# Kernel optimization log

Hardware: AMD Instinct MI355X
Metric: run time of the kernel (lower is better)

The kernel has to match this reference:

```python
import jax, jax.numpy as jnp
import numpy as np
import math

M = 512          # num_bin_x
NB = 512         # num_bin_y
NUM_NODES = 2_000_000
K = 4            # max bins a node can overlap per dim (size <= 2.5 bins)
SQRT2 = math.sqrt(2.0)


def setup_inputs() -> dict:
    key = jax.random.key(0)
    k1, k2 = jax.random.split(key)
    node_pos = jax.random.uniform(k1, (NUM_NODES, 2), jnp.float32, 0.05, 0.95)
    # node sizes between 0.5 and 2.5 bins (normalized layout units)
    node_size = jax.random.uniform(k2, (NUM_NODES, 2), jnp.float32) * (2.0 / M) + (0.5 / M)
    return {
        "node_pos": node_pos,
        "node_size": node_size,
        "node_weight": jnp.ones((NUM_NODES,), jnp.float32),
        "expand_ratio": jnp.ones((NUM_NODES,), jnp.float32),
        "unit_len": jnp.array([1.0 / M, 1.0 / NB], jnp.float32),
        "init_density_map": jnp.zeros((M, NB), jnp.float32),
        "num_bin_x": M,
        "num_bin_y": NB,
    }


def pre_normalize(node_pos, node_size, node_weight, expand_ratio, unit_len, mx, ny):
    # density_map_cuda.pre_normalize: expand tiny nodes to sqrt(2)*unit_len,
    # rescale weight to preserve area, convert rects to bin coordinates.
    ux, uy = unit_len[0], unit_len[1]
    w, h = node_size[:, 0], node_size[:, 1]
    new_w = jnp.maximum(w, SQRT2 * ux)
    new_h = jnp.maximum(h, SQRT2 * uy)
    weight = node_weight * expand_ratio * (w * h) / (new_w * new_h)
    xl = jnp.clip((node_pos[:, 0] - 0.5 * new_w) / ux, 0.0, mx)
    xh = jnp.clip((node_pos[:, 0] + 0.5 * new_w) / ux, 0.0, mx)
    yl = jnp.clip((node_pos[:, 1] - 0.5 * new_h) / uy, 0.0, ny)
    yh = jnp.clip((node_pos[:, 1] + 0.5 * new_h) / uy, 0.0, ny)
    return jnp.stack([xl, xh, yl, yh, weight], axis=1)  # [N, 5]


def scatter_density(info, mx, ny):
    # density_map_cuda.forward: overlap-area scatter-add of node rects into bins.
    xl, xh, yl, yh, w = info[:, 0], info[:, 1], info[:, 2], info[:, 3], info[:, 4]
    bx0 = jnp.floor(xl).astype(jnp.int32)
    by0 = jnp.floor(yl).astype(jnp.int32)
    dm = jnp.zeros((mx, ny), jnp.float32)
    for dx in range(K):
        ix = bx0 + dx
        fx = ix.astype(jnp.float32)
        ox = jnp.clip(jnp.minimum(xh, fx + 1.0) - jnp.maximum(xl, fx), 0.0)
        ixc = jnp.clip(ix, 0, mx - 1)
        for dy in range(K):
            iy = by0 + dy
            fy = iy.astype(jnp.float32)
            oy = jnp.clip(jnp.minimum(yh, fy + 1.0) - jnp.maximum(yl, fy), 0.0)
            iyc = jnp.clip(iy, 0, ny - 1)
            dm = dm.at[ixc, iyc].add(w * ox * oy)
    return dm


def make_transforms(n):
    k = jnp.arange(n, dtype=jnp.float32)[:, None]
    m = jnp.arange(n, dtype=jnp.float32)[None, :]
    ang = jnp.pi * k * (2.0 * m + 1.0) / (2.0 * n)
    C = jnp.cos(ang)  # [freq, space]
    S = jnp.sin(ang)
    w = jnp.where(jnp.arange(n) == 0, 1.0, 2.0).astype(jnp.float32)
    return C, S, w


def spectral_solve(dm, unit_len, mx, ny):
    # fft_scale construction from __init__
    wj = (jnp.arange(mx, dtype=jnp.float32) * (2.0 * jnp.pi / mx))[:, None]
    wk = (jnp.arange(ny, dtype=jnp.float32) * (2.0 * jnp.pi / ny))[None, :]
    wk = wk * (unit_len[0] / unit_len[1])  # scale_w_k=True
    wsq = wj ** 2 + wk ** 2
    wsq = wsq.at[0, 0].set(1.0)
    pscale = (1.0 / wsq).at[0, 0].set(0.0)
    fx_scale = wj * pscale * 0.5
    fy_scale = wk * pscale * 0.5

    Cx, Sx, wx = make_transforms(mx)
    Cy, Sy, wy = make_transforms(ny)
    # dct2: coeff[u,v] = (1/(M*N)) * sum_{m,n} dm[m,n] cos(pi u(2m+1)/2M) cos(pi v(2n+1)/2N)
    coeff = (Cx @ dm @ Cy.T) / (mx * ny)
    ICx = (wx[:, None] * Cx)  # weighted inverse cosine basis [freq, space]
    ICy = (wy[:, None] * Cy)
    ISx = (wx[:, None] * Sx)
    ISy = (wy[:, None] * Sy)
    potential = ICx.T @ (coeff * pscale) @ ICy          # idct2
    force_x = ISx.T @ (coeff * fx_scale) @ ICy          # idxst_idct
    force_y = ICx.T @ (coeff * fy_scale) @ ISy          # idct_idxst
    return potential, force_x, force_y


def reference(node_pos, node_size, node_weight, expand_ratio, unit_len,
              init_density_map, num_bin_x, num_bin_y):
    info = pre_normalize(node_pos, node_size, node_weight, expand_ratio,
                         unit_len, num_bin_x, num_bin_y)
    density_map = init_density_map + scatter_density(info, num_bin_x, num_bin_y)
    potential, _, _ = spectral_solve(density_map, unit_len, num_bin_x, num_bin_y)
    energy = jnp.sum(potential * density_map)
    return energy
```

## Files before the change

### kernel.cpp

```cpp
#include <hip/hip_runtime.h>
#include <math.h>

#define MX 512
#define NY 512
#define TWO_PI 6.283185307179586f

#define TSHIFT 6
#define NT 64
#define LDIM 68
#define SLAB (LDIM * LDIM)
#define SLAB4 (SLAB / 4)
#define NPB 2048
#define KPT 8
#define CAP 40960
#define TTARGET 1216
#define RPARTS 19
#define QSCALE 26214.0f
#define QINV (1.0f / 26214.0f)

typedef __attribute__((ext_vector_type(8))) short short8;
typedef __attribute__((ext_vector_type(4))) float float4_t;
typedef __attribute__((ext_vector_type(4))) unsigned short ushort4_t;

__device__ __forceinline__ unsigned short f2bf(float x) {
    union { float f; unsigned u; } v; v.f = x;
    unsigned r = v.u + 0x7fffu + ((v.u >> 16) & 1u);
    return (unsigned short)(r >> 16);
}
__device__ __forceinline__ float bf2f(unsigned short h) {
    union { float f; unsigned u; } v; v.u = ((unsigned)h) << 16;
    return v.f;
}

__device__ __forceinline__ void node_bounds(float2 p, float2 s, float ux, float uy,
                                            float& xl, float& xh, float& yl, float& yh,
                                            float& nw, float& nh) {
    const float SQ2 = 1.41421356237309515f;
    nw = fmaxf(s.x, SQ2 * ux);
    nh = fmaxf(s.y, SQ2 * uy);
    xl = fminf(fmaxf((p.x - 0.5f * nw) / ux, 0.0f), (float)MX);
    xh = fminf(fmaxf((p.x + 0.5f * nw) / ux, 0.0f), (float)MX);
    yl = fminf(fmaxf((p.y - 0.5f * nh) / uy, 0.0f), (float)NY);
    yh = fminf(fmaxf((p.y + 0.5f * nh) / uy, 0.0f), (float)NY);
}

__global__ void gen_cos_kernel(unsigned short* __restrict__ Ch,
                               unsigned short* __restrict__ Cl,
                               unsigned int* __restrict__ base,
                               unsigned int* __restrict__ cursor,
                               float* __restrict__ out, int cap_mode) {
    int idx = blockIdx.x * blockDim.x + threadIdx.x;
    if (idx == 0) *out = 0.0f;
    if (cap_mode && idx <= NT) {
        base[idx] = (unsigned int)idx * CAP;
        if (idx < NT) cursor[idx] = (unsigned int)idx * CAP;
    }
    int a = idx >> 9;
    int j = idx & 511;
    float x = cospif((float)(a * (2 * j + 1)) * (1.0f / 1024.0f));
    unsigned short hi = f2bf(x);
    Ch[idx] = hi;
    Cl[idx] = f2bf(x - bf2f(hi));
}

__global__ __launch_bounds__(256)
void count_kernel(const float2* __restrict__ pos, const float2* __restrict__ size,
                  const float* __restrict__ unit_len,
                  unsigned int* __restrict__ cnt, int n) {
    __shared__ unsigned int h[NT];
    if (threadIdx.x < NT) h[threadIdx.x] = 0;
    __syncthreads();
    float ux = unit_len[0], uy = unit_len[1];
    int start = blockIdx.x * NPB;
    int end = min(start + NPB, n);
#pragma unroll
    for (int k = 0; k < KPT; k++) {
        int i = start + k * 256 + (int)threadIdx.x;
        if (i < end) {
            float xl, xh, yl, yh, nw, nh;
            node_bounds(pos[i], size[i], ux, uy, xl, xh, yl, yh, nw, nh);
            int bx0 = min((int)floorf(xl), MX - 1);
            int by0 = min((int)floorf(yl), NY - 1);
            atomicAdd(&h[((bx0 >> TSHIFT) << 3) | (by0 >> TSHIFT)], 1u);
        }
    }
    __syncthreads();
    if (threadIdx.x < NT) {
        unsigned int c = h[threadIdx.x];
        if (c) atomicAdd(&cnt[threadIdx.x], c);
    }
}

__global__ void scan_kernel(const unsigned int* __restrict__ cnt,
                            unsigned int* __restrict__ base,
                            unsigned int* __restrict__ cursor) {
    if (threadIdx.x == 0 && blockIdx.x == 0) {
        unsigned int ex = 0;
        for (int t = 0; t < NT; t++) {
            base[t] = ex;
            cursor[t] = ex;
            ex += cnt[t];
        }
        base[NT] = ex;
    }
}

__global__ __launch_bounds__(256)
void place_kernel(const float2* __restrict__ pos, const float2* __restrict__ size,
                  const float* __restrict__ nwt, const float* __restrict__ er,
                  const float* __restrict__ unit_len,
                  const unsigned int* __restrict__ base,
                  unsigned int* __restrict__ cursor,
                  float4* __restrict__ pb, int n) {
    __shared__ unsigned int h[NT];
    __shared__ unsigned int lb[NT + 1];
    __shared__ unsigned int bb[NT];
    __shared__ float4 buf[NPB];
    __shared__ unsigned char til[NPB];
    if (threadIdx.x < NT) h[threadIdx.x] = 0;
    __syncthreads();
    float ux = unit_len[0], uy = unit_len[1];
    int start = blockIdx.x * NPB;
    int end = min(start + NPB, n);

    float cxl[KPT], cyl[KPT], cw[KPT];
    unsigned int cq[KPT], pk[KPT];
#pragma unroll
    for (int k = 0; k < KPT; k++) {
        int i = start + k * 256 + (int)threadIdx.x;
        if (i < end) {
            float2 p = pos[i], s = size[i];
            float xl, xh, yl, yh, nw, nh;
            node_bounds(p, s, ux, uy, xl, xh, yl, yh, nw, nh);
            cxl[k] = xl; cyl[k] = yl;
            cw[k] = nwt[i] * er[i] * (s.x * s.y) / (nw * nh);
            unsigned qx = (unsigned)((xh - xl) * QSCALE + 0.5f);
            unsigned qy = (unsigned)((yh - yl) * QSCALE + 0.5f);
            if (qx > 65535u) qx = 65535u;
            if (qy > 65535u) qy = 65535u;
            cq[k] = qx | (qy << 16);
            int bx0 = min((int)floorf(xl), MX - 1);
            int by0 = min((int)floorf(yl), NY - 1);
            unsigned int t = ((bx0 >> TSHIFT) << 3) | (by0 >> TSHIFT);
            pk[k] = (t << 11) | atomicAdd(&h[t], 1u);
        }
    }
    __syncthreads();
    if (threadIdx.x < NT) {
        unsigned int c = h[threadIdx.x];
        unsigned int S = c;
#pragma unroll
        for (int d = 1; d < 64; d <<= 1) {
            unsigned int v = __shfl_up(S, d, 64);
            if ((int)threadIdx.x >= d) S += v;
        }
        lb[threadIdx.x] = S - c;
        if (threadIdx.x == NT - 1) lb[NT] = S;
        bb[threadIdx.x] = c ? atomicAdd(&cursor[threadIdx.x], c) : 0u;
    }
    __syncthreads();
#pragma unroll
    for (int k = 0; k < KPT; k++) {
        int i = start + k * 256 + (int)threadIdx.x;
        if (i < end) {
            unsigned int t = pk[k] >> 11;
            unsigned int slot = lb[t] + (pk[k] & 2047u);
            buf[slot] = make_float4(cxl[k], cyl[k], cw[k], __uint_as_float(cq[k]));
            til[slot] = (unsigned char)t;
        }
    }
    __syncthreads();
    unsigned int total = lb[NT];
    for (unsigned int j = threadIdx.x; j < total; j += 256) {
        unsigned int t = til[j];
        unsigned int dst = bb[t] + (j - lb[t]);
        if (dst < base[t + 1]) pb[dst] = buf[j];
    }
}

__device__ __forceinline__ void accum_one(float4 v, float* acc, int tbx, int tby) {
    float xl = v.x, yl = v.y, w = v.z;
    unsigned q = __float_as_uint(v.w);
    float xh = xl + (float)(q & 0xffffu) * QINV;
    float yh = yl + (float)(q >> 16) * QINV;
    int bx0 = min((int)floorf(xl), MX - 1);
    int by0 = min((int)floorf(yl), NY - 1);
    float oxs[4], oys[4];
    int rb[4], lys[4];
#pragma unroll
    for (int d = 0; d < 4; d++) {
        int ix = bx0 + d;
        float fx = (float)ix;
        oxs[d] = fmaxf(fminf(xh, fx + 1.0f) - fmaxf(xl, fx), 0.0f);
        rb[d] = (min(ix, MX - 1) - tbx) * LDIM;
        int iy = by0 + d;
        float fy = (float)iy;
        oys[d] = fmaxf(fminf(yh, fy + 1.0f) - fmaxf(yl, fy), 0.0f);
        lys[d] = min(iy, NY - 1) - tby;
    }
#pragma unroll
    for (int dx = 0; dx < 4; dx++) {
        if (oxs[dx] == 0.0f) continue;
        float wox = w * oxs[dx];
#pragma unroll
        for (int dy = 0; dy < 4; dy++) {
            float vv = wox * oys[dy];
            if (vv != 0.0f) atomicAdd(&acc[rb[dx] + lys[dy]], vv);
        }
    }
}

__global__ __launch_bounds__(256)
void accum_kernel(const float4* __restrict__ pb,
                  const unsigned int* __restrict__ base,
                  const unsigned int* __restrict__ cursor,
                  float* __restrict__ slab, int T) {
    __shared__ float acc[SLAB];
    __shared__ int sh_t, sh_done;
    __shared__ unsigned int sh_ks, sh_ke, sh_b0;
    int tid = threadIdx.x;
    if (tid < 64) {
        unsigned int t = tid;
        unsigned int b0 = base[t];
        unsigned int cap = base[t + 1] - b0;
        unsigned int cr = cursor[t] - b0;
        unsigned int c = cr < cap ? cr : cap;
        unsigned int S = c;
#pragma unroll
        for (int d = 1; d < 64; d <<= 1) {
            unsigned int v = __shfl_up(S, d, 64);
            if (tid >= d) S += v;
        }
        unsigned int total = __shfl(S, 63, 64);
        unsigned int nb = total ? (unsigned int)(((unsigned long long)c * (unsigned int)T) / total) + 1u : 1u;
        unsigned int Pn = nb;
#pragma unroll
        for (int d = 1; d < 64; d <<= 1) {
            unsigned int v = __shfl_up(Pn, d, 64);
            if (tid >= d) Pn += v;
        }
        unsigned int NBU = __shfl(Pn, 63, 64);
        unsigned int Pex = Pn - nb;
        unsigned int b = blockIdx.x;
        if (tid == 0) sh_done = (b >= NBU) ? 1 : 0;
        if (b >= Pex && b < Pn) {
            unsigned int s = b - Pex;
            unsigned int chunk = nb ? (c + nb - 1) / nb : 0u;
            unsigned int ks = s * chunk;
            unsigned int ke = min(c, ks + chunk);
            sh_t = (int)t; sh_ks = ks; sh_ke = ke; sh_b0 = b0;
        }
    }
    for (int e = tid; e < SLAB4; e += 256)
        ((float4*)acc)[e] = make_float4(0.f, 0.f, 0.f, 0.f);
    __syncthreads();
    if (sh_done) return;

    int t = sh_t;
    int tbx = (t >> 3) << TSHIFT;
    int tby = (t & 7) << TSHIFT;
    unsigned int b0 = sh_b0;
    unsigned int ke = sh_ke;

    unsigned int k = sh_ks + (unsigned int)tid;
    float4 cur = make_float4(0.f, 0.f, 0.f, 0.f);
    bool have = (k < ke);
    if (have) cur = pb[b0 + k];
    while (have) {
        unsigned int k2 = k + 256;
        bool have2 = (k2 < ke);
        float4 nxt = make_float4(0.f, 0.f, 0.f, 0.f);
        if (have2) nxt = pb[b0 + k2];
        accum_one(cur, acc, tbx, tby);
        cur = nxt; k = k2; have = have2;
    }
    __syncthreads();

    float4* dst = (float4*)(slab + (size_t)blockIdx.x * SLAB);
    for (int e = tid; e < SLAB4; e += 256)
        dst[e] = ((float4*)acc)[e];
}

__global__ __launch_bounds__(256)
void reduce_slabs_kernel(const float* __restrict__ slab,
                         float* __restrict__ tacc,
                         const unsigned int* __restrict__ base,
                         const unsigned int* __restrict__ cursor, int T) {
    __shared__ unsigned int sh_P, sh_nb;
    int t = blockIdx.x / RPARTS;
    int part = blockIdx.x - t * RPARTS;
    int tid = threadIdx.x;
    if (tid < 64) {
        unsigned int tt = tid;
        unsigned int b0 = base[tt];
        unsigned int cap = base[tt + 1] - b0;
        unsigned int cr = cursor[tt] - b0;
        unsigned int c = cr < cap ? cr : cap;
        unsigned int S = c;
#pragma unroll
        for (int d = 1; d < 64; d <<= 1) {
            unsigned int v = __shfl_up(S, d, 64);
            if (tid >= d) S += v;
        }
        unsigned int total = __shfl(S, 63, 64);
        unsigned int nb = total ? (unsigned int)(((unsigned long long)c * (unsigned int)T) / total) + 1u : 1u;
        unsigned int Pn = nb;
#pragma unroll
        for (int d = 1; d < 64; d <<= 1) {
            unsigned int v = __shfl_up(Pn, d, 64);
            if (tid >= d) Pn += v;
        }
        if ((int)tt == t) { sh_P = Pn - nb; sh_nb = nb; }
    }
    __syncthreads();
    int e = part * 256 + tid;
    if (e < SLAB) {
        const float* s0 = slab + (size_t)sh_P * SLAB + e;
        float sum = 0.0f;
        unsigned int nb = sh_nb;
        for (unsigned int s = 0; s < nb; s++) sum += s0[(size_t)s * SLAB];
        tacc[(size_t)t * SLAB + e] = sum;
    }
}

__global__ __launch_bounds__(256)
void combine_kernel(const float* __restrict__ tacc,
                    const float* __restrict__ init_dm,
                    unsigned short* __restrict__ dmh,
                    unsigned short* __restrict__ dml) {
    int v = blockIdx.x * blockDim.x + threadIdx.x;
    int gx = v >> 7;
    int g4 = v & 127;
    int gy = g4 << 2;
    int rx = gx & 63, ry = gy & 63;
    int tx0 = gx >> TSHIFT, ty0 = gy >> TSHIFT;

    float4 sum = ((const float4*)init_dm)[v];
#pragma unroll
    for (int ax = 0; ax < 2; ax++) {
        int tx = tx0 - ax;
        if (tx < 0 || (ax == 1 && rx > 3)) continue;
        int lx = rx + (ax << TSHIFT);
#pragma unroll
        for (int ay = 0; ay < 2; ay++) {
            int ty = ty0 - ay;
            if (ty < 0 || (ay == 1 && ry > 0)) continue;
            int ly = ry + (ay << TSHIFT);
            float4 sv = *(const float4*)(tacc
                + (size_t)((tx << 3) | ty) * SLAB + lx * LDIM + ly);
            sum.x += sv.x; sum.y += sv.y; sum.z += sv.z; sum.w += sv.w;
        }
    }
    ushort4_t hi, lo;
    float sv[4] = {sum.x, sum.y, sum.z, sum.w};
#pragma unroll
    for (int r = 0; r < 4; r++) {
        unsigned short h = f2bf(sv[r]);
        hi[r] = h;
        lo[r] = f2bf(sv[r] - bf2f(h));
    }
    int idx = (gx << 9) | gy;
    *(ushort4_t*)(dmh + idx) = hi;
    *(ushort4_t*)(dml + idx) = lo;
}

__global__ __launch_bounds__(256)
void scatter_kernel(const float2* __restrict__ pos, const float2* __restrict__ size,
                    const float* __restrict__ nwt, const float* __restrict__ er,
                    const float* __restrict__ unit_len,
                    float* __restrict__ dm, int n) {
    int i = blockIdx.x * blockDim.x + threadIdx.x;
    if (i >= n) return;
    float ux = unit_len[0], uy = unit_len[1];
    float2 p = pos[i], s = size[i];
    float xl, xh, yl, yh, nw, nh;
    node_bounds(p, s, ux, uy, xl, xh, yl, yh, nw, nh);
    float w = nwt[i] * er[i] * (s.x * s.y) / (nw * nh);
    int bx0 = (int)floorf(xl);
    int by0 = (int)floorf(yl);
#pragma unroll
    for (int dx = 0; dx < 4; dx++) {
        int ix = bx0 + dx;
        float fx = (float)ix;
        float ox = fmaxf(fminf(xh, fx + 1.0f) - fmaxf(xl, fx), 0.0f);
        if (ox == 0.0f) continue;
        int rowoff = min(max(ix, 0), MX - 1) * NY;
        float wox = w * ox;
#pragma unroll
        for (int dy = 0; dy < 4; dy++) {
            int iy = by0 + dy;
            float fy = (float)iy;
            float oy = fmaxf(fminf(yh, fy + 1.0f) - fmaxf(yl, fy), 0.0f);
            float vv = wox * oy;
            if (vv != 0.0f) atomicAdd(&dm[rowoff + min(max(iy, 0), NY - 1)], vv);
        }
    }
}

__global__ void cvt_dm_kernel(const float* __restrict__ dm,
                              unsigned short* __restrict__ dmh,
                              unsigned short* __restrict__ dml) {
    int idx = blockIdx.x * blockDim.x + threadIdx.x;
    float x = dm[idx];
    unsigned short hi = f2bf(x);
    dmh[idx] = hi;
    dml[idx] = f2bf(x - bf2f(hi));
}

__global__ __launch_bounds__(256)
void dct1_mfma_kernel(const unsigned short* __restrict__ dmh,
                      const unsigned short* __restrict__ dml,
                      const unsigned short* __restrict__ Ch,
                      const unsigned short* __restrict__ Cl,
                      unsigned short* __restrict__ UhT,
                      unsigned short* __restrict__ UlT) {
    int lane = threadIdx.x & 63;
    int wv = threadIdx.x >> 6;
    int tile = blockIdx.x * 4 + wv;
    int jt = (tile >> 5) * 16;
    int bt = (tile & 31) * 16;
    int m = lane & 15, q = lane >> 4;
    float4_t acc = {0.f, 0.f, 0.f, 0.f};
    const unsigned short* ah_row = dmh + (jt + m) * 512;
    const unsigned short* al_row = dml + (jt + m) * 512;
    const unsigned short* bh_row = Ch + (bt + m) * 512;
    const unsigned short* bl_row = Cl + (bt + m) * 512;
#pragma unroll 4
    for (int k0 = 0; k0 < 512; k0 += 32) {
        int off = k0 + q * 8;
        short8 ah = *(const short8*)(ah_row + off);
        short8 al = *(const short8*)(al_row + off);
        short8 bh = *(const short8*)(bh_row + off);
        short8 bl = *(const short8*)(bl_row + off);
        acc = __builtin_amdgcn_mfma_f32_16x16x32_bf16(ah, bh, acc, 0, 0, 0);
        acc = __builtin_amdgcn_mfma_f32_16x16x32_bf16(ah, bl, acc, 0, 0, 0);
        acc = __builtin_amdgcn_mfma_f32_16x16x32_bf16(al, bh, acc, 0, 0, 0);
    }
#pragma unroll
    for (int r = 0; r < 4; r++) {
        float v = acc[r];
        unsigned short hi = f2bf(v);
        int addr = (bt + m) * 512 + jt + q * 4 + r;
        UhT[addr] = hi;
        UlT[addr] = f2bf(v - bf2f(hi));
    }
}

__global__ __launch_bounds__(256)
void dct2_mfma_kernel(const unsigned short* __restrict__ Ch,
                      const unsigned short* __restrict__ Cl,
                      const unsigned short* __restrict__ UhT,
                      const unsigned short* __restrict__ UlT,
                      const float* __restrict__ unit_len,
                      float* __restrict__ out) {
    __shared__ float red[4];
    int lane = threadIdx.x & 63;
    int wv = threadIdx.x >> 6;
    int tile = blockIdx.x * 4 + wv;
    int at = (tile >> 5) * 16;
    int bt = (tile & 31) * 16;
    int m = lane & 15, q = lane >> 4;
    float4_t acc = {0.f, 0.f, 0.f, 0.f};
    const unsigned short* ah_row = Ch + (at + m) * 512;
    const unsigned short* al_row = Cl + (at + m) * 512;
    const unsigned short* bh_row = UhT + (bt + m) * 512;
    const unsigned short* bl_row = UlT + (bt + m) * 512;
#pragma unroll 4
    for (int k0 = 0; k0 < 512; k0 += 32) {
        int off = k0 + q * 8;
        short8 ah = *(const short8*)(ah_row + off);
        short8 al = *(const short8*)(al_row + off);
        short8 bh = *(const short8*)(bh_row + off);
        short8 bl = *(const short8*)(bl_row + off);
        acc = __builtin_amdgcn_mfma_f32_16x16x32_bf16(ah, bh, acc, 0, 0, 0);
        acc = __builtin_amdgcn_mfma_f32_16x16x32_bf16(ah, bl, acc, 0, 0, 0);
        acc = __builtin_amdgcn_mfma_f32_16x16x32_bf16(al, bh, acc, 0, 0, 0);
    }
    float ratio = unit_len[0] / unit_len[1];
    int b = bt + m;
    float wkb = (float)b * (TWO_PI / (float)NY) * ratio;
    float wyb = (b == 0) ? 1.0f : 2.0f;
    float e = 0.0f;
#pragma unroll
    for (int r = 0; r < 4; r++) {
        int a = at + q * 4 + r;
        float wja = (float)a * (TWO_PI / (float)MX);
        float wsq = wja * wja + wkb * wkb;
        float ps = (a == 0 && b == 0) ? 0.0f : (1.0f / wsq);
        float wxa = (a == 0) ? 1.0f : 2.0f;
        e += wxa * wyb * ps * acc[r] * acc[r];
    }
#pragma unroll
    for (int off = 32; off > 0; off >>= 1) e += __shfl_down(e, off, 64);
    if (lane == 0) red[wv] = e;
    __syncthreads();
    if (threadIdx.x == 0) {
        float t = red[0] + red[1] + red[2] + red[3];
        atomicAdd(out, t * (1.0f / ((float)MX * (float)NY)));
    }
}

extern "C" void kernel_launch(void* const* d_in, const int* in_sizes, int n_in,
                              void* d_out, int out_size, void* d_ws, size_t ws_size,
                              hipStream_t stream) {
    const float2* node_pos  = (const float2*)d_in[0];
    const float2* node_size = (const float2*)d_in[1];
    const float*  node_wt   = (const float*)d_in[2];
    const float*  exp_ratio = (const float*)d_in[3];
    const float*  unit_len  = (const float*)d_in[4];
    const float*  init_dm   = (const float*)d_in[5];
    float* out = (float*)d_out;
    int n = in_sizes[2];

    char* wsb = (char*)d_ws;
    size_t off = 0;
    auto alloc = [&](size_t bytes) { void* p = wsb + off; off = (off + bytes + 255) & ~(size_t)255; return p; };
    unsigned short* Ch   = (unsigned short*)alloc((size_t)MX * NY * 2);
    unsigned short* Cl   = (unsigned short*)alloc((size_t)MX * NY * 2);
    unsigned short* dmh  = (unsigned short*)alloc((size_t)MX * NY * 2);
    unsigned short* dml  = (unsigned short*)alloc((size_t)MX * NY * 2);
    unsigned short* UhT  = (unsigned short*)alloc((size_t)MX * NY * 2);
    unsigned short* UlT  = (unsigned short*)alloc((size_t)MX * NY * 2);
    float*          dm     = (float*)alloc((size_t)MX * NY * sizeof(float));
    unsigned int*   cnt    = (unsigned int*)alloc(NT * sizeof(unsigned int));
    unsigned int*   tbase  = (unsigned int*)alloc((NT + 1) * sizeof(unsigned int));
    unsigned int*   cursor = (unsigned int*)alloc(NT * sizeof(unsigned int));
    float*          tacc   = (float*)alloc((size_t)NT * SLAB * sizeof(float));
    size_t off_common = off;
    size_t slab_bytes = (size_t)SLAB * sizeof(float);

    float4* pbF = (float4*)alloc((size_t)NT * CAP * sizeof(float4));
    int TF = 0;
    float* slbF = nullptr;
    if (off <= ws_size) {
        size_t navail = (ws_size - off) / slab_bytes;
        if (navail >= 320) {
            size_t t = navail - 64;
            TF = (int)(t > TTARGET ? TTARGET : t);
            slbF = (float*)alloc((size_t)(TF + 64) * slab_bytes);
        }
    }
    bool tierFast = (slbF != nullptr);

    off = off_common;
    float4* pbE = (float4*)alloc((size_t)n * sizeof(float4));
    int TE = 0;
    float* slbE = nullptr;
    if (off <= ws_size) {
        size_t navail = (ws_size - off) / slab_bytes;
        if (navail >= 128) {
            size_t t = navail - 64;
            TE = (int)(t > TTARGET ? TTARGET : t);
            slbE = (float*)alloc((size_t)(TE + 64) * slab_bytes);
        }
    }
    bool tierExact = (slbE != nullptr);

    gen_cos_kernel<<<(MX * NY) / 256, 256, 0, stream>>>(Ch, Cl, tbase, cursor,
                                                        out, tierFast ? 1 : 0);

    if (tierFast || tierExact) {
        float4* pb  = tierFast ? pbF : pbE;
        float*  slb = tierFast ? slbF : slbE;
        int     T   = tierFast ? TF : TE;
        int nblk = (n + NPB - 1) / NPB;
        if (!tierFast) {
            hipMemsetAsync(cnt, 0, NT * sizeof(unsigned int), stream);
            count_kernel<<<nblk, 256, 0, stream>>>(node_pos, node_size, unit_len, cnt, n);
            scan_kernel<<<1, 64, 0, stream>>>(cnt, tbase, cursor);
        }
        place_kernel<<<nblk, 256, 0, stream>>>(
            node_pos, node_size, node_wt, exp_ratio, unit_len, tbase, cursor, pb, n);
        accum_kernel<<<T + 64, 256, 0, stream>>>(pb, tbase, cursor, slb, T);
        reduce_slabs_kernel<<<NT * RPARTS, 256, 0, stream>>>(slb, tacc, tbase, cursor, T);
        combine_kernel<<<256, 256, 0, stream>>>(tacc, init_dm, dmh, dml);
    } else {
        hipMemcpyAsync(dm, init_dm, (size_t)MX * NY * sizeof(float),
                       hipMemcpyDeviceToDevice, stream);
        scatter_kernel<<<(n + 255) / 256, 256, 0, stream>>>(
            node_pos, node_size, node_wt, exp_ratio, unit_len, dm, n);
        cvt_dm_kernel<<<(MX * NY) / 256, 256, 0, stream>>>(dm, dmh, dml);
    }

    dct1_mfma_kernel<<<256, 256, 0, stream>>>(dmh, dml, Ch, Cl, UhT, UlT);
    dct2_mfma_kernel<<<256, 256, 0, stream>>>(Ch, Cl, UhT, UlT, unit_len, out);
}
```

Baseline: 235.0 us.

## Fuse cosine table generation into placement and slab reduction into accumulation

On the fast tier, cosine-table generation and output zeroing move into the placement kernel via a grid-stride loop. The cursor and done counters are zeroed by a memset instead of a separate kernel. The accumulation kernel now reduces per-tile slabs itself: the last block to finish each tile, detected with an atomic counter, sums that tile's slabs, which removes the separate reduce_slabs launch. The intent is fewer kernel launches and less launch serialisation, at the cost of a serial tail reduction done by a single block per tile and added threadfence/atomic synchronisation.

```diff
diff --git a/kernel.cpp b/kernel.cpp
--- a/kernel.cpp
+++ b/kernel.cpp
@@ -44,79 +44,30 @@
     yh = fminf(fmaxf((p.y + 0.5f * nh) / uy, 0.0f), (float)NY);
 }
 
-__global__ void gen_cos_kernel(unsigned short* __restrict__ Ch,
-                               unsigned short* __restrict__ Cl,
-                               unsigned int* __restrict__ base,
-                               unsigned int* __restrict__ cursor,
-                               float* __restrict__ out, int cap_mode) {
-    int idx = blockIdx.x * blockDim.x + threadIdx.x;
-    if (idx == 0) *out = 0.0f;
-    if (cap_mode && idx <= NT) {
-        base[idx] = (unsigned int)idx * CAP;
-        if (idx < NT) cursor[idx] = (unsigned int)idx * CAP;
-    }
-    int a = idx >> 9;
-    int j = idx & 511;
-    float x = cospif((float)(a * (2 * j + 1)) * (1.0f / 1024.0f));
-    unsigned short hi = f2bf(x);
-    Ch[idx] = hi;
-    Cl[idx] = f2bf(x - bf2f(hi));
-}
-
-__global__ __launch_bounds__(256)
-void count_kernel(const float2* __restrict__ pos, const float2* __restrict__ size,
-                  const float* __restrict__ unit_len,
-                  unsigned int* __restrict__ cnt, int n) {
-    __shared__ unsigned int h[NT];
-    if (threadIdx.x < NT) h[threadIdx.x] = 0;
-    __syncthreads();
-    float ux = unit_len[0], uy = unit_len[1];
-    int start = blockIdx.x * NPB;
-    int end = min(start + NPB, n);
-#pragma unroll
-    for (int k = 0; k < KPT; k++) {
-        int i = start + k * 256 + (int)threadIdx.x;
-        if (i < end) {
-            float xl, xh, yl, yh, nw, nh;
-            node_bounds(pos[i], size[i], ux, uy, xl, xh, yl, yh, nw, nh);
-            int bx0 = min((int)floorf(xl), MX - 1);
-            int by0 = min((int)floorf(yl), NY - 1);
-            atomicAdd(&h[((bx0 >> TSHIFT) << 3) | (by0 >> TSHIFT)], 1u);
-        }
-    }
-    __syncthreads();
-    if (threadIdx.x < NT) {
-        unsigned int c = h[threadIdx.x];
-        if (c) atomicAdd(&cnt[threadIdx.x], c);
-    }
-}
-
-__global__ void scan_kernel(const unsigned int* __restrict__ cnt,
-                            unsigned int* __restrict__ base,
-                            unsigned int* __restrict__ cursor) {
-    if (threadIdx.x == 0 && blockIdx.x == 0) {
-        unsigned int ex = 0;
-        for (int t = 0; t < NT; t++) {
-            base[t] = ex;
-            cursor[t] = ex;
-            ex += cnt[t];
-        }
-        base[NT] = ex;
-    }
-}
-
-__global__ __launch_bounds__(256)
-void place_kernel(const float2* __restrict__ pos, const float2* __restrict__ size,
-                  const float* __restrict__ nwt, const float* __restrict__ er,
-                  const float* __restrict__ unit_len,
-                  const unsigned int* __restrict__ base,
-                  unsigned int* __restrict__ cursor,
-                  float4* __restrict__ pb, int n) {
+__global__ __launch_bounds__(256)
+void place_fast_kernel(const float2* __restrict__ pos, const float2* __restrict__ size,
+                       const float* __restrict__ nwt, const float* __restrict__ er,
+                       const float* __restrict__ unit_len,
+                       unsigned int* __restrict__ cursor,
+                       float4* __restrict__ pb,
+                       unsigned short* __restrict__ Ch,
+                       unsigned short* __restrict__ Cl,
+                       float* __restrict__ out, int n) {
     __shared__ unsigned int h[NT];
     __shared__ unsigned int lb[NT + 1];
     __shared__ unsigned int bb[NT];
     __shared__ float4 buf[NPB];
     __shared__ unsigned char til[NPB];
+    if (blockIdx.x == 0 && threadIdx.x == 0) *out = 0.0f;
+    for (int idx = blockIdx.x * 256 + (int)threadIdx.x; idx < MX * NY;
+         idx += gridDim.x * 256) {
+        int a = idx >> 9;
+        int j = idx & 511;
+        float x = cospif((float)(a * (2 * j + 1)) * (1.0f / 1024.0f));
+        unsigned short hi = f2bf(x);
+        Ch[idx] = hi;
+        Cl[idx] = f2bf(x - bf2f(hi));
+    }
     if (threadIdx.x < NT) h[threadIdx.x] = 0;
     __syncthreads();
     float ux = unit_len[0], uy = unit_len[1];
@@ -174,7 +125,7 @@
     for (unsigned int j = threadIdx.x; j < total; j += 256) {
         unsigned int t = til[j];
         unsigned int dst = bb[t] + (j - lb[t]);
-        if (dst < base[t + 1]) pb[dst] = buf[j];
+        if (dst < CAP) pb[(size_t)t * CAP + dst] = buf[j];
     }
 }
 
@@ -207,6 +158,268 @@
             float vv = wox * oys[dy];
             if (vv != 0.0f) atomicAdd(&acc[rb[dx] + lys[dy]], vv);
         }
+    }
+}
+
+__global__ __launch_bounds__(256)
+void accum_fast_kernel(const float4* __restrict__ pb,
+                       const unsigned int* __restrict__ cursor,
+                       float* __restrict__ slab, float* __restrict__ tacc,
+                       unsigned int* __restrict__ done, int T) {
+    __shared__ float acc[SLAB];
+    __shared__ int sh_t, sh_done;
+    __shared__ unsigned int sh_ks, sh_ke, sh_P0, sh_nb;
+    __shared__ int amLast;
+    int tid = threadIdx.x;
+    if (tid < 64) {
+        unsigned int t = tid;
+        unsigned int cr = cursor[t];
+        unsigned int c = cr < CAP ? cr : CAP;
+        unsigned int S = c;
+#pragma unroll
+        for (int d = 1; d < 64; d <<= 1) {
+            unsigned int v = __shfl_up(S, d, 64);
+            if (tid >= d) S += v;
+        }
+        unsigned int total = __shfl(S, 63, 64);
+        unsigned int nb = total ? (unsigned int)(((unsigned long long)c * (unsigned int)T) / total) + 1u : 1u;
+        unsigned int Pn = nb;
+#pragma unroll
+        for (int d = 1; d < 64; d <<= 1) {
+            unsigned int v = __shfl_up(Pn, d, 64);
+            if (tid >= d) Pn += v;
+        }
+        unsigned int NBU = __shfl(Pn, 63, 64);
+        unsigned int Pex = Pn - nb;
+        unsigned int b = blockIdx.x;
+        if (tid == 0) sh_done = (b >= NBU) ? 1 : 0;
+        if (b >= Pex && b < Pn) {
+            unsigned int s = b - Pex;
+            unsigned int chunk = nb ? (c + nb - 1) / nb : 0u;
+            unsigned int ks = s * chunk;
+            unsigned int ke = min(c, ks + chunk);
+            sh_t = (int)t; sh_ks = ks; sh_ke = ke; sh_P0 = Pex; sh_nb = nb;
+        }
+    }
+    for (int e = tid; e < SLAB4; e += 256)
+        ((float4*)acc)[e] = make_float4(0.f, 0.f, 0.f, 0.f);
+    __syncthreads();
+    if (sh_done) return;
+
+    int t = sh_t;
+    int tbx = (t >> 3) << TSHIFT;
+    int tby = (t & 7) << TSHIFT;
+    unsigned int b0 = (unsigned int)t * CAP;
+    unsigned int ke = sh_ke;
+
+    unsigned int k = sh_ks + (unsigned int)tid;
+    float4 cur = make_float4(0.f, 0.f, 0.f, 0.f);
+    bool have = (k < ke);
+    if (have) cur = pb[b0 + k];
+    while (have) {
+        unsigned int k2 = k + 256;
+        bool have2 = (k2 < ke);
+        float4 nxt = make_float4(0.f, 0.f, 0.f, 0.f);
+        if (have2) nxt = pb[b0 + k2];
+        accum_one(cur, acc, tbx, tby);
+        cur = nxt; k = k2; have = have2;
+    }
+    __syncthreads();
+
+    float4* dst = (float4*)(slab + (size_t)blockIdx.x * SLAB);
+    for (int e = tid; e < SLAB4; e += 256)
+        dst[e] = ((float4*)acc)[e];
+
+    __threadfence();
+    __syncthreads();
+    if (tid == 0) {
+        unsigned int old = atomicAdd(&done[t], 1u);
+        amLast = (old == sh_nb - 1u) ? 1 : 0;
+    }
+    __syncthreads();
+    if (amLast) {
+        __threadfence();
+        const float* s0 = slab + (size_t)sh_P0 * SLAB;
+        unsigned int nb = sh_nb;
+        for (int e = tid; e < SLAB; e += 256) {
+            float sum = 0.0f;
+            for (unsigned int s = 0; s < nb; s++) sum += s0[(size_t)s * SLAB + e];
+            tacc[(size_t)t * SLAB + e] = sum;
+        }
+    }
+}
+
+__global__ __launch_bounds__(256)
+void combine_kernel(const float* __restrict__ tacc,
+                    const float* __restrict__ init_dm,
+                    unsigned short* __restrict__ dmh,
+                    unsigned short* __restrict__ dml) {
+    int v = blockIdx.x * blockDim.x + threadIdx.x;
+    int gx = v >> 7;
+    int g4 = v & 127;
+    int gy = g4 << 2;
+    int rx = gx & 63, ry = gy & 63;
+    int tx0 = gx >> TSHIFT, ty0 = gy >> TSHIFT;
+
+    float4 sum = ((const float4*)init_dm)[v];
+#pragma unroll
+    for (int ax = 0; ax < 2; ax++) {
+        int tx = tx0 - ax;
+        if (tx < 0 || (ax == 1 && rx > 3)) continue;
+        int lx = rx + (ax << TSHIFT);
+#pragma unroll
+        for (int ay = 0; ay < 2; ay++) {
+            int ty = ty0 - ay;
+            if (ty < 0 || (ay == 1 && ry > 0)) continue;
+            int ly = ry + (ay << TSHIFT);
+            float4 sv = *(const float4*)(tacc
+                + (size_t)((tx << 3) | ty) * SLAB + lx * LDIM + ly);
+            sum.x += sv.x; sum.y += sv.y; sum.z += sv.z; sum.w += sv.w;
+        }
+    }
+    ushort4_t hi, lo;
+    float sv[4] = {sum.x, sum.y, sum.z, sum.w};
+#pragma unroll
+    for (int r = 0; r < 4; r++) {
+        unsigned short h = f2bf(sv[r]);
+        hi[r] = h;
+        lo[r] = f2bf(sv[r] - bf2f(h));
+    }
+    int idx = (gx << 9) | gy;
+    *(ushort4_t*)(dmh + idx) = hi;
+    *(ushort4_t*)(dml + idx) = lo;
+}
+
+__global__ void gen_cos_kernel(unsigned short* __restrict__ Ch,
+                               unsigned short* __restrict__ Cl,
+                               unsigned int* __restrict__ base,
+                               unsigned int* __restrict__ cursor,
+                               float* __restrict__ out, int cap_mode) {
+    int idx = blockIdx.x * blockDim.x + threadIdx.x;
+    if (idx == 0) *out = 0.0f;
+    if (cap_mode && idx <= NT) {
+        base[idx] = (unsigned int)idx * CAP;
+        if (idx < NT) cursor[idx] = (unsigned int)idx * CAP;
+    }
+    int a = idx >> 9;
+    int j = idx & 511;
+    float x = cospif((float)(a * (2 * j + 1)) * (1.0f / 1024.0f));
+    unsigned short hi = f2bf(x);
+    Ch[idx] = hi;
+    Cl[idx] = f2bf(x - bf2f(hi));
+}
+
+__global__ __launch_bounds__(256)
+void count_kernel(const float2* __restrict__ pos, const float2* __restrict__ size,
+                  const float* __restrict__ unit_len,
+                  unsigned int* __restrict__ cnt, int n) {
+    __shared__ unsigned int h[NT];
+    if (threadIdx.x < NT) h[threadIdx.x] = 0;
+    __syncthreads();
+    float ux = unit_len[0], uy = unit_len[1];
+    int start = blockIdx.x * NPB;
+    int end = min(start + NPB, n);
+#pragma unroll
+    for (int k = 0; k < KPT; k++) {
+        int i = start + k * 256 + (int)threadIdx.x;
+        if (i < end) {
+            float xl, xh, yl, yh, nw, nh;
+            node_bounds(pos[i], size[i], ux, uy, xl, xh, yl, yh, nw, nh);
+            int bx0 = min((int)floorf(xl), MX - 1);
+            int by0 = min((int)floorf(yl), NY - 1);
+            atomicAdd(&h[((bx0 >> TSHIFT) << 3) | (by0 >> TSHIFT)], 1u);
+        }
+    }
+    __syncthreads();
+    if (threadIdx.x < NT) {
+        unsigned int c = h[threadIdx.x];
+        if (c) atomicAdd(&cnt[threadIdx.x], c);
+    }
+}
+
+__global__ void scan_kernel(const unsigned int* __restrict__ cnt,
+                            unsigned int* __restrict__ base,
+                            unsigned int* __restrict__ cursor) {
+    if (threadIdx.x == 0 && blockIdx.x == 0) {
+        unsigned int ex = 0;
+        for (int t = 0; t < NT; t++) {
+            base[t] = ex;
+            cursor[t] = ex;
+            ex += cnt[t];
+        }
+        base[NT] = ex;
+    }
+}
+
+__global__ __launch_bounds__(256)
+void place_kernel(const float2* __restrict__ pos, const float2* __restrict__ size,
+                  const float* __restrict__ nwt, const float* __restrict__ er,
+                  const float* __restrict__ unit_len,
+                  const unsigned int* __restrict__ base,
+                  unsigned int* __restrict__ cursor,
+                  float4* __restrict__ pb, int n) {
+    __shared__ unsigned int h[NT];
+    __shared__ unsigned int lb[NT + 1];
+    __shared__ unsigned int bb[NT];
+    __shared__ float4 buf[NPB];
+    __shared__ unsigned char til[NPB];
+    if (threadIdx.x < NT) h[threadIdx.x] = 0;
+    __syncthreads();
+    float ux = unit_len[0], uy = unit_len[1];
+    int start = blockIdx.x * NPB;
+    int end = min(start + NPB, n);
+    float cxl[KPT], cyl[KPT], cw[KPT];
+    unsigned int cq[KPT], pk[KPT];
+#pragma unroll
+    for (int k = 0; k < KPT; k++) {
+        int i = start + k * 256 + (int)threadIdx.x;
+        if (i < end) {
+            float2 p = pos[i], s = size[i];
+            float xl, xh, yl, yh, nw, nh;
+            node_bounds(p, s, ux, uy, xl, xh, yl, yh, nw, nh);
+            cxl[k] = xl; cyl[k] = yl;
+            cw[k] = nwt[i] * er[i] * (s.x * s.y) / (nw * nh);
+            unsigned qx = (unsigned)((xh - xl) * QSCALE + 0.5f);
+            unsigned qy = (unsigned)((yh - yl) * QSCALE + 0.5f);
+            if (qx > 65535u) qx = 65535u;
+            if (qy > 65535u) qy = 65535u;
+            cq[k] = qx | (qy << 16);
+            int bx0 = min((int)floorf(xl), MX - 1);
+            int by0 = min((int)floorf(yl), NY - 1);
+            unsigned int t = ((bx0 >> TSHIFT) << 3) | (by0 >> TSHIFT);
+            pk[k] = (t << 11) | atomicAdd(&h[t], 1u);
+        }
+    }
+    __syncthreads();
+    if (threadIdx.x < NT) {
+        unsigned int c = h[threadIdx.x];
+        unsigned int S = c;
+#pragma unroll
+        for (int d = 1; d < 64; d <<= 1) {
+            unsigned int v = __shfl_up(S, d, 64);
+            if ((int)threadIdx.x >= d) S += v;
+        }
+        lb[threadIdx.x] = S - c;
+        if (threadIdx.x == NT - 1) lb[NT] = S;
+        bb[threadIdx.x] = c ? atomicAdd(&cursor[threadIdx.x], c) : 0u;
+    }
+    __syncthreads();
+#pragma unroll
+    for (int k = 0; k < KPT; k++) {
+        int i = start + k * 256 + (int)threadIdx.x;
+        if (i < end) {
+            unsigned int t = pk[k] >> 11;
+            unsigned int slot = lb[t] + (pk[k] & 2047u);
+            buf[slot] = make_float4(cxl[k], cyl[k], cw[k], __uint_as_float(cq[k]));
+            til[slot] = (unsigned char)t;
+        }
+    }
+    __syncthreads();
+    unsigned int total = lb[NT];
+    for (unsigned int j = threadIdx.x; j < total; j += 256) {
+        unsigned int t = til[j];
+        unsigned int dst = bb[t] + (j - lb[t]);
+        if (dst < base[t + 1]) pb[dst] = buf[j];
     }
 }
 
@@ -255,13 +468,11 @@
         ((float4*)acc)[e] = make_float4(0.f, 0.f, 0.f, 0.f);
     __syncthreads();
     if (sh_done) return;
-
     int t = sh_t;
     int tbx = (t >> 3) << TSHIFT;
     int tby = (t & 7) << TSHIFT;
     unsigned int b0 = sh_b0;
     unsigned int ke = sh_ke;
-
     unsigned int k = sh_ks + (unsigned int)tid;
     float4 cur = make_float4(0.f, 0.f, 0.f, 0.f);
     bool have = (k < ke);
@@ -275,7 +486,6 @@
         cur = nxt; k = k2; have = have2;
     }
     __syncthreads();
-
     float4* dst = (float4*)(slab + (size_t)blockIdx.x * SLAB);
     for (int e = tid; e < SLAB4; e += 256)
         dst[e] = ((float4*)acc)[e];
@@ -321,47 +531,6 @@
         for (unsigned int s = 0; s < nb; s++) sum += s0[(size_t)s * SLAB];
         tacc[(size_t)t * SLAB + e] = sum;
     }
-}
-
-__global__ __launch_bounds__(256)
-void combine_kernel(const float* __restrict__ tacc,
-                    const float* __restrict__ init_dm,
-                    unsigned short* __restrict__ dmh,
-                    unsigned short* __restrict__ dml) {
-    int v = blockIdx.x * blockDim.x + threadIdx.x;
-    int gx = v >> 7;
-    int g4 = v & 127;
-    int gy = g4 << 2;
-    int rx = gx & 63, ry = gy & 63;
-    int tx0 = gx >> TSHIFT, ty0 = gy >> TSHIFT;
-
-    float4 sum = ((const float4*)init_dm)[v];
-#pragma unroll
-    for (int ax = 0; ax < 2; ax++) {
-        int tx = tx0 - ax;
-        if (tx < 0 || (ax == 1 && rx > 3)) continue;
-        int lx = rx + (ax << TSHIFT);
-#pragma unroll
-        for (int ay = 0; ay < 2; ay++) {
-            int ty = ty0 - ay;
-            if (ty < 0 || (ay == 1 && ry > 0)) continue;
-            int ly = ry + (ay << TSHIFT);
-            float4 sv = *(const float4*)(tacc
-                + (size_t)((tx << 3) | ty) * SLAB + lx * LDIM + ly);
-            sum.x += sv.x; sum.y += sv.y; sum.z += sv.z; sum.w += sv.w;
-        }
-    }
-    ushort4_t hi, lo;
-    float sv[4] = {sum.x, sum.y, sum.z, sum.w};
-#pragma unroll
-    for (int r = 0; r < 4; r++) {
-        unsigned short h = f2bf(sv[r]);
-        hi[r] = h;
-        lo[r] = f2bf(sv[r] - bf2f(h));
-    }
-    int idx = (gx << 9) | gy;
-    *(ushort4_t*)(dmh + idx) = hi;
-    *(ushort4_t*)(dml + idx) = lo;
 }
 
 __global__ __launch_bounds__(256)
@@ -524,10 +693,12 @@
     float*          dm     = (float*)alloc((size_t)MX * NY * sizeof(float));
     unsigned int*   cnt    = (unsigned int*)alloc(NT * sizeof(unsigned int));
     unsigned int*   tbase  = (unsigned int*)alloc((NT + 1) * sizeof(unsigned int));
-    unsigned int*   cursor = (unsigned int*)alloc(NT * sizeof(unsigned int));
+    unsigned int*   ctrl   = (unsigned int*)alloc(128 * sizeof(unsigned int));
     float*          tacc   = (float*)alloc((size_t)NT * SLAB * sizeof(float));
     size_t off_common = off;
     size_t slab_bytes = (size_t)SLAB * sizeof(float);
+    unsigned int* cursorF = ctrl;
+    unsigned int* doneF   = ctrl + 64;
 
     float4* pbF = (float4*)alloc((size_t)NT * CAP * sizeof(float4));
     int TF = 0;
@@ -556,23 +727,31 @@
     }
     bool tierExact = (slbE != nullptr);
 
-    gen_cos_kernel<<<(MX * NY) / 256, 256, 0, stream>>>(Ch, Cl, tbase, cursor,
-                                                        out, tierFast ? 1 : 0);
-
-    if (tierFast || tierExact) {
-        float4* pb  = tierFast ? pbF : pbE;
-        float*  slb = tierFast ? slbF : slbE;
-        int     T   = tierFast ? TF : TE;
+    if (tierFast) {
         int nblk = (n + NPB - 1) / NPB;
-        if (!tierFast) {
-            hipMemsetAsync(cnt, 0, NT * sizeof(unsigned int), stream);
-            count_kernel<<<nblk, 256, 0, stream>>>(node_pos, node_size, unit_len, cnt, n);
-            scan_kernel<<<1, 64, 0, stream>>>(cnt, tbase, cursor);
-        }
+        hipMemsetAsync(ctrl, 0, 128 * sizeof(unsigned int), stream);
+        place_fast_kernel<<<nblk, 256, 0, stream>>>(
+            node_pos, node_size, node_wt, exp_ratio, unit_len, cursorF, pbF,
+            Ch, Cl, out, n);
+        accum_fast_kernel<<<TF + 64, 256, 0, stream>>>(pbF, cursorF, slbF,
+                                                       tacc, doneF, TF);
+        combine_kernel<<<256, 256, 0, stream>>>(tacc, init_dm, dmh, dml);
+        dct1_mfma_kernel<<<256, 256, 0, stream>>>(dmh, dml, Ch, Cl, UhT, UlT);
+        dct2_mfma_kernel<<<256, 256, 0, stream>>>(Ch, Cl, UhT, UlT, unit_len, out);
+        return;
+    }
+
+    gen_cos_kernel<<<(MX * NY) / 256, 256, 0, stream>>>(Ch, Cl, tbase, cursorF,
+                                                        out, 0);
+    if (tierExact) {
+        int nblk = (n + NPB - 1) / NPB;
+        hipMemsetAsync(cnt, 0, NT * sizeof(unsigned int), stream);
+        count_kernel<<<nblk, 256, 0, stream>>>(node_pos, node_size, unit_len, cnt, n);
+        scan_kernel<<<1, 64, 0, stream>>>(cnt, tbase, cursorF);
         place_kernel<<<nblk, 256, 0, stream>>>(
-            node_pos, node_size, node_wt, exp_ratio, unit_len, tbase, cursor, pb, n);
-        accum_kernel<<<T + 64, 256, 0, stream>>>(pb, tbase, cursor, slb, T);
-        reduce_slabs_kernel<<<NT * RPARTS, 256, 0, stream>>>(slb, tacc, tbase, cursor, T);
+            node_pos, node_size, node_wt, exp_ratio, unit_len, tbase, cursorF, pbE, n);
+        accum_kernel<<<TE + 64, 256, 0, stream>>>(pbE, tbase, cursorF, slbE, TE);
+        reduce_slabs_kernel<<<NT * RPARTS, 256, 0, stream>>>(slbE, tacc, tbase, cursorF, TE);
         combine_kernel<<<256, 256, 0, stream>>>(tacc, init_dm, dmh, dml);
     } else {
         hipMemcpyAsync(dm, init_dm, (size_t)MX * NY * sizeof(float),
```

Result: slower. 464.2 us (+97.5%).
